# Optimization experiments

Hardware: AMD Instinct MI355X
Metric: run time of the kernel (lower is better)

Reference implementation:

```python
import jax, jax.numpy as jnp
import numpy as np

K = 9          # kernel_size
PAD = 4        # padding
N_OUT, C_IN = 32, 32


def setup_inputs() -> dict:
    key = jax.random.key(0)
    k1, k2, k3, k4, k5 = jax.random.split(key, 5)
    x = jax.random.normal(k1, (16, C_IN, 192, 192), jnp.float32)
    sx = jax.random.uniform(k2, (N_OUT, C_IN), jnp.float32, 0.2, 4.0)
    sy = jax.random.uniform(k3, (N_OUT, C_IN), jnp.float32, 0.2, 4.0)
    th = jax.random.uniform(k4, (N_OUT, C_IN), jnp.float32, 0.0, 2.0 * np.pi)
    weight = jnp.stack([sx, sy, th], axis=-1)          # [N, C, 3]
    bias = jax.random.normal(k5, (N_OUT,), jnp.float32) * 0.01
    return {"x": x, "weight": weight, "bias": bias}


def _gaussian_kernels(weight, k):
    # weight: [N, C, 3] -> normalized anisotropic Gaussian kernels [N, C, k, k]
    sx, sy = weight[..., 0], weight[..., 1]
    rad = weight[..., 2] / 180.0 * jnp.pi          # matches theta/180*pi in source
    c, s = jnp.cos(rad), jnp.sin(rad)
    sx2, sy2 = sx * sx, sy * sy
    # Sigma = U diag(sx^2, sy^2) U^T, U = [[c,-s],[s,c]] -> Sigma = [[a,b],[b,d]]
    a = c * c * sx2 + s * s * sy2
    b = c * s * (sx2 - sy2)
    d = s * s * sx2 + c * c * sy2
    det = a * d - b * b
    ia, ib, id_ = d / det, -b / det, a / det       # closed-form 2x2 inverse
    ax = jnp.arange(k, dtype=jnp.float32) - k // 2
    xx = ax[None, :]                               # x varies along columns
    yy = ax[:, None]                               # y varies along rows
    # quadratic form: ia*x^2 + 2*ib*x*y + id*y^2, broadcast to [N, C, k, k]
    q = (ia[..., None, None] * (xx * xx)
         + 2.0 * ib[..., None, None] * (xx * yy)
         + id_[..., None, None] * (yy * yy))
    ker = jnp.exp(-0.5 * q)
    return ker / jnp.sum(ker, axis=(-2, -1), keepdims=True)


def reference(x, weight, bias):
    w = _gaussian_kernels(weight, K)               # [N, C, K, K]
    out = jax.lax.conv_general_dilated(
        x, w, window_strides=(1, 1), padding=[(PAD, PAD), (PAD, PAD)],
        dimension_numbers=("NCHW", "OIHW", "NCHW"))
    return out + bias[None, :, None, None]
```

## Files before the change

### kernel.cpp

```cpp
#include <hip/hip_runtime.h>

#define H 192
#define W 192
#define CIN 32
#define NOUT 32
#define NB 16
#define PADI 4

#define HT 16
#define WTL 16
#define RROWS 24
#define RCOLS 24

typedef __attribute__((ext_vector_type(8))) short bf16x8;
typedef __attribute__((ext_vector_type(4))) float f32x4;

__device__ __forceinline__ unsigned short f2bf(float f) {
    union { float f; unsigned int u; } v; v.f = f;
    unsigned int r = v.u + 0x7fffu + ((v.u >> 16) & 1u);
    return (unsigned short)(r >> 16);
}

__global__ void genw_kernel(const float* __restrict__ wp, unsigned short* __restrict__ W2g) {
    const int b = blockIdx.x;
    const int o = b >> 5;
    const int i = b & 31;
    const int t = threadIdx.x;

    float sx = wp[b * 3 + 0], sy = wp[b * 3 + 1], th = wp[b * 3 + 2];
    float rad = th / 180.0f * 3.14159265358979323846f;
    float co = cosf(rad), si = sinf(rad);
    float sx2 = sx * sx, sy2 = sy * sy;
    float a = co * co * sx2 + si * si * sy2;
    float bb = co * si * (sx2 - sy2);
    float d = si * si * sx2 + co * co * sy2;
    float det = a * d - bb * bb;
    float ia = d / det, ib = -bb / det, idd = a / det;

    const int tap = t;
    float e = 0.0f;
    if (tap < 81) {
        float xx = (float)(tap % 9 - 4);
        float yy = (float)(tap / 9 - 4);
        float q = ia * xx * xx + 2.0f * ib * xx * yy + idd * yy * yy;
        e = expf(-0.5f * q);
    }
    float s = e;
    #pragma unroll
    for (int off = 32; off > 0; off >>= 1) s += __shfl_down(s, off);
    __shared__ float ws[2];
    if ((t & 63) == 0) ws[t >> 6] = s;
    __syncthreads();
    float total = ws[0] + ws[1];

    if (tap < 81) {
        int mt = o >> 4, m = o & 15, quad = i >> 3, j = i & 7;
        W2g[((((mt * 81 + tap) * 4 + quad) * 16 + m) << 3) + j] = f2bf(e / total);
    }
}

__global__ __launch_bounds__(256, 4) void conv_kernel(
    const float* __restrict__ x, const unsigned short* __restrict__ W2g,
    const float* __restrict__ bias, float* __restrict__ out)
{
    __shared__ __align__(16) unsigned short ldsx[4 * RROWS * RCOLS * 8];

    const int t = threadIdx.x;
    const int bid = (blockIdx.x & 7) * 288 + (blockIdx.x >> 3);
    const int wb = bid % (W / WTL);
    const int hb = (bid / (W / WTL)) % (H / HT);
    const int n  = bid / ((W / WTL) * (H / HT));
    const int row0 = hb * HT - PADI;
    const int col0 = wb * WTL - PADI;
    const float* xn = x + (size_t)n * CIN * H * W;

    float v[9][8];
    #pragma unroll
    for (int it = 0; it < 9; ++it) {
        int idx = it * 256 + t;
        int w = idx % RCOLS;
        int r = (idx / RCOLS) % RROWS;
        int quad = idx / (RCOLS * RROWS);
        int row = row0 + r, col = col0 + w;
        #pragma unroll
        for (int k = 0; k < 8; k++) v[it][k] = 0.0f;
        if ((unsigned)row < (unsigned)H && (unsigned)col < (unsigned)W) {
            const float* p = xn + ((size_t)(quad * 8) * H + row) * W + col;
            #pragma unroll
            for (int k = 0; k < 8; k++) v[it][k] = p[(size_t)k * H * W];
        }
    }
    #pragma unroll
    for (int it = 0; it < 9; ++it) {
        int idx = it * 256 + t;
        unsigned int d[4];
        #pragma unroll
        for (int k = 0; k < 4; k++)
            d[k] = (unsigned int)f2bf(v[it][2 * k]) | ((unsigned int)f2bf(v[it][2 * k + 1]) << 16);
        *(uint4*)&ldsx[(size_t)idx * 8] = make_uint4(d[0], d[1], d[2], d[3]);
    }

    const int wave = t >> 6;
    const int lane = t & 63;
    const int l15 = lane & 15;
    const int quad4 = lane >> 4;
    const int mt = wave & 1;
    const int rbase = (wave >> 1) * 8;

    const bf16x8* __restrict__ Wp = (const bf16x8*)W2g;

    bf16x8 A[2][9];
    #pragma unroll
    for (int dy = 0; dy < 9; dy++)
        A[0][dy] = Wp[((mt * 81 + dy * 9 + 0) * 4 + quad4) * 16 + l15];

    __syncthreads();

    f32x4 acc[8];
    #pragma unroll
    for (int i = 0; i < 8; i++) acc[i] = (f32x4){0.f, 0.f, 0.f, 0.f};

    const unsigned short* bptr = &ldsx[(size_t)(((quad4 * RROWS + rbase) * RCOLS) + l15) * 8];

    #pragma unroll
    for (int dx = 0; dx < 9; dx++) {
        const int cur = dx & 1, nxt = cur ^ 1;
        if (dx < 8) {
            #pragma unroll
            for (int dy = 0; dy < 9; dy++)
                A[nxt][dy] = Wp[((mt * 81 + dy * 9 + (dx + 1)) * 4 + quad4) * 16 + l15];
        }
        #pragma unroll
        for (int rr = 0; rr < 16; rr++) {
            const bf16x8 bfrag = *(const bf16x8*)&bptr[(size_t)(rr * RCOLS + dx) * 8];
            #pragma unroll
            for (int dy = 0; dy < 9; dy++) {
                const int orr = rr - dy;
                if (orr >= 0 && orr < 8) {
                    acc[orr] = __builtin_amdgcn_mfma_f32_16x16x32_bf16(
                        A[cur][dy], bfrag, acc[orr], 0, 0, 0);
                }
            }
        }
    }

    float* outn = out + (size_t)n * NOUT * H * W;
    float bb[4];
    #pragma unroll
    for (int reg = 0; reg < 4; reg++) bb[reg] = bias[mt * 16 + quad4 * 4 + reg];
    #pragma unroll
    for (int orr = 0; orr < 8; orr++) {
        const int row = hb * HT + rbase + orr;
        const int col = wb * WTL + l15;
        #pragma unroll
        for (int reg = 0; reg < 4; reg++) {
            const int och = mt * 16 + quad4 * 4 + reg;
            outn[((size_t)och * H + row) * W + col] = acc[orr][reg] + bb[reg];
        }
    }
}

extern "C" void kernel_launch(void* const* d_in, const int* in_sizes, int n_in,
                              void* d_out, int out_size, void* d_ws, size_t ws_size,
                              hipStream_t stream) {
    const float* x    = (const float*)d_in[0];
    const float* wp   = (const float*)d_in[1];
    const float* bias = (const float*)d_in[2];
    float* out = (float*)d_out;
    unsigned short* W2g = (unsigned short*)d_ws;

    genw_kernel<<<NOUT * CIN, 128, 0, stream>>>(wp, W2g);
    const int blocks = NB * (H / HT) * (W / WTL);
    conv_kernel<<<blocks, 256, 0, stream>>>(x, W2g, bias, out);
}
```

Baseline: 190.2 us.

## Pre-pad and convert input to bf16 NHWC, load tiles via global_load_lds

A new prep kernel converts the fp32 NCHW input into a zero-padded bf16 channel-interleaved buffer in workspace, and also generates the Gaussian weights in the same launch. The conv kernel then fills LDS with direct global-to-LDS 16-byte loads, with no bounds checks or per-tile conversion. This removes the repeated halo reads and fp32-to-bf16 conversion done in every tile. In exchange it adds an extra full pass over the input and roughly 41 MB of workspace writes and reads. The old path remains as a fallback when the workspace is too small.

Result: no change. 192.5 us (+1.2%).

```diff
diff --git a/kernel.cpp b/kernel.cpp
--- a/kernel.cpp
+++ b/kernel.cpp
@@ -1,4 +1,5 @@
 #include <hip/hip_runtime.h>
+#include <stdint.h>
 
 #define H 192
 #define W 192
@@ -9,11 +10,15 @@
 
 #define HT 16
 #define WTL 16
-#define RROWS 24
-#define RCOLS 24
+#define RR 24
+#define RC 24
+#define PADW 200
 
 typedef __attribute__((ext_vector_type(8))) short bf16x8;
 typedef __attribute__((ext_vector_type(4))) float f32x4;
+
+typedef __attribute__((address_space(1))) const void gvoid;
+typedef __attribute__((address_space(3))) void svoid;
 
 __device__ __forceinline__ unsigned short f2bf(float f) {
     union { float f; unsigned int u; } v; v.f = f;
@@ -21,12 +26,12 @@
     return (unsigned short)(r >> 16);
 }
 
-__global__ void genw_kernel(const float* __restrict__ wp, unsigned short* __restrict__ W2g) {
-    const int b = blockIdx.x;
+__device__ __forceinline__ void genw_body(int b, int t, int nthr,
+                                          const float* __restrict__ wp,
+                                          unsigned short* __restrict__ W2g,
+                                          float* ws ) {
     const int o = b >> 5;
     const int i = b & 31;
-    const int t = threadIdx.x;
-
     float sx = wp[b * 3 + 0], sy = wp[b * 3 + 1], th = wp[b * 3 + 2];
     float rad = th / 180.0f * 3.14159265358979323846f;
     float co = cosf(rad), si = sinf(rad);
@@ -48,10 +53,10 @@
     float s = e;
     #pragma unroll
     for (int off = 32; off > 0; off >>= 1) s += __shfl_down(s, off);
-    __shared__ float ws[2];
     if ((t & 63) == 0) ws[t >> 6] = s;
     __syncthreads();
-    float total = ws[0] + ws[1];
+    float total = 0.0f;
+    for (int k = 0; k < nthr / 64; k++) total += ws[k];
 
     if (tap < 81) {
         int mt = o >> 4, m = o & 15, quad = i >> 3, j = i & 7;
@@ -59,11 +64,131 @@
     }
 }
 
+__global__ void prep_kernel(const float* __restrict__ x, const float* __restrict__ wp,
+                            unsigned short* __restrict__ W2g,
+                            unsigned short* __restrict__ xpad) {
+    __shared__ float ws[4];
+    if (blockIdx.x < 10000) {
+        int gid = blockIdx.x * 256 + threadIdx.x;
+        int q = gid & 3;
+        int pix = gid >> 2;
+        int pw = pix % PADW;
+        int rest = pix / PADW;
+        int pr = rest % PADW;
+        int n = rest / PADW;
+        int r = pr - PADI, c = pw - PADI;
+        unsigned int d[4] = {0u, 0u, 0u, 0u};
+        if ((unsigned)r < (unsigned)H && (unsigned)c < (unsigned)W) {
+            const float* p = x + (((size_t)n * CIN + q * 8) * H + r) * W + c;
+            #pragma unroll
+            for (int k = 0; k < 4; k++) {
+                float v0 = p[(size_t)(2 * k) * H * W];
+                float v1 = p[(size_t)(2 * k + 1) * H * W];
+                d[k] = (unsigned int)f2bf(v0) | ((unsigned int)f2bf(v1) << 16);
+            }
+        }
+        *(uint4*)(xpad + (size_t)gid * 8) = make_uint4(d[0], d[1], d[2], d[3]);
+    } else {
+        genw_body(blockIdx.x - 10000, threadIdx.x, 256, wp, W2g, ws);
+    }
+}
+
+__global__ void genw_kernel(const float* __restrict__ wp, unsigned short* __restrict__ W2g) {
+    __shared__ float ws[2];
+    genw_body(blockIdx.x, threadIdx.x, 128, wp, W2g, ws);
+}
+
 __global__ __launch_bounds__(256, 4) void conv_kernel(
+    const unsigned short* __restrict__ xpad, const unsigned short* __restrict__ W2g,
+    const float* __restrict__ bias, float* __restrict__ out)
+{
+    __shared__ __align__(16) unsigned short ldsx[4 * RR * RC * 8];
+
+    const int t = threadIdx.x;
+    const int bid = (blockIdx.x & 7) * 288 + (blockIdx.x >> 3);
+    const int wb = bid % (W / WTL);
+    const int hb = (bid / (W / WTL)) % (H / HT);
+    const int n  = bid / ((W / WTL) * (H / HT));
+    const int wave = t >> 6;
+    const int lane = t & 63;
+
+    {
+        const size_t pixbase = ((size_t)n * PADW + hb * HT) * PADW + wb * WTL;
+        const unsigned short* srcq = xpad + pixbase * 32 + wave * 8;
+        #pragma unroll
+        for (int k = 0; k < 9; k++) {
+            int rem = k * 64 + lane;
+            int r = rem / RC;
+            int w = rem - r * RC;
+            const unsigned short* src = srcq + ((size_t)r * PADW + w) * 32;
+            char* dst = (char*)ldsx + ((size_t)(wave * 576 + k * 64) * 16);
+            __builtin_amdgcn_global_load_lds((gvoid*)src, (svoid*)dst, 16, 0, 0);
+        }
+    }
+
+    const int l15 = lane & 15;
+    const int quad4 = lane >> 4;
+    const int mt = wave & 1;
+    const int rbase = (wave >> 1) * 8;
+
+    const bf16x8* __restrict__ Wp = (const bf16x8*)W2g;
+
+    bf16x8 A[2][9];
+    #pragma unroll
+    for (int dy = 0; dy < 9; dy++)
+        A[0][dy] = Wp[((mt * 81 + dy * 9 + 0) * 4 + quad4) * 16 + l15];
+
+    __syncthreads();
+
+    f32x4 acc[8];
+    #pragma unroll
+    for (int i = 0; i < 8; i++) acc[i] = (f32x4){0.f, 0.f, 0.f, 0.f};
+
+    const unsigned short* bptr = &ldsx[(size_t)(((quad4 * RR + rbase) * RC) + l15) * 8];
+
+    #pragma unroll
+    for (int dx = 0; dx < 9; dx++) {
+        const int cur = dx & 1, nxt = cur ^ 1;
+        if (dx < 8) {
+            #pragma unroll
+            for (int dy = 0; dy < 9; dy++)
+                A[nxt][dy] = Wp[((mt * 81 + dy * 9 + (dx + 1)) * 4 + quad4) * 16 + l15];
+        }
+        #pragma unroll
+        for (int rr = 0; rr < 16; rr++) {
+            const bf16x8 bfrag = *(const bf16x8*)&bptr[(size_t)(rr * RC + dx) * 8];
+            #pragma unroll
+            for (int dy = 0; dy < 9; dy++) {
+                const int orr = rr - dy;
+                if (orr >= 0 && orr < 8) {
+                    acc[orr] = __builtin_amdgcn_mfma_f32_16x16x32_bf16(
+                        A[cur][dy], bfrag, acc[orr], 0, 0, 0);
+                }
+            }
+        }
+    }
+
+    float* outn = out + (size_t)n * NOUT * H * W;
+    float bb[4];
+    #pragma unroll
+    for (int reg = 0; reg < 4; reg++) bb[reg] = bias[mt * 16 + quad4 * 4 + reg];
+    #pragma unroll
+    for (int orr = 0; orr < 8; orr++) {
+        const int row = hb * HT + rbase + orr;
+        const int col = wb * WTL + l15;
+        #pragma unroll
+        for (int reg = 0; reg < 4; reg++) {
+            const int och = mt * 16 + quad4 * 4 + reg;
+            outn[((size_t)och * H + row) * W + col] = acc[orr][reg] + bb[reg];
+        }
+    }
+}
+
+__global__ __launch_bounds__(256, 4) void conv_fb(
     const float* __restrict__ x, const unsigned short* __restrict__ W2g,
     const float* __restrict__ bias, float* __restrict__ out)
 {
-    __shared__ __align__(16) unsigned short ldsx[4 * RROWS * RCOLS * 8];
+    __shared__ __align__(16) unsigned short ldsx[4 * RR * RC * 8];
 
     const int t = threadIdx.x;
     const int bid = (blockIdx.x & 7) * 288 + (blockIdx.x >> 3);
@@ -78,9 +203,9 @@
     #pragma unroll
     for (int it = 0; it < 9; ++it) {
         int idx = it * 256 + t;
-        int w = idx % RCOLS;
-        int r = (idx / RCOLS) % RROWS;
-        int quad = idx / (RCOLS * RROWS);
+        int w = idx % RC;
+        int r = (idx / RC) % RR;
+        int quad = idx / (RC * RR);
         int row = row0 + r, col = col0 + w;
         #pragma unroll
         for (int k = 0; k < 8; k++) v[it][k] = 0.0f;
@@ -108,7 +233,6 @@
     const int rbase = (wave >> 1) * 8;
 
     const bf16x8* __restrict__ Wp = (const bf16x8*)W2g;
-
     bf16x8 A[2][9];
     #pragma unroll
     for (int dy = 0; dy < 9; dy++)
@@ -120,7 +244,7 @@
     #pragma unroll
     for (int i = 0; i < 8; i++) acc[i] = (f32x4){0.f, 0.f, 0.f, 0.f};
 
-    const unsigned short* bptr = &ldsx[(size_t)(((quad4 * RROWS + rbase) * RCOLS) + l15) * 8];
+    const unsigned short* bptr = &ldsx[(size_t)(((quad4 * RR + rbase) * RC) + l15) * 8];
 
     #pragma unroll
     for (int dx = 0; dx < 9; dx++) {
@@ -132,7 +256,7 @@
         }
         #pragma unroll
         for (int rr = 0; rr < 16; rr++) {
-            const bf16x8 bfrag = *(const bf16x8*)&bptr[(size_t)(rr * RCOLS + dx) * 8];
+            const bf16x8 bfrag = *(const bf16x8*)&bptr[(size_t)(rr * RC + dx) * 8];
             #pragma unroll
             for (int dy = 0; dy < 9; dy++) {
                 const int orr = rr - dy;
@@ -167,9 +291,19 @@
     const float* wp   = (const float*)d_in[1];
     const float* bias = (const float*)d_in[2];
     float* out = (float*)d_out;
-    unsigned short* W2g = (unsigned short*)d_ws;
-
-    genw_kernel<<<NOUT * CIN, 128, 0, stream>>>(wp, W2g);
+
+    const size_t W2G_BYTES  = 165888;
+    const size_t XPAD_BYTES = (size_t)NB * PADW * PADW * CIN * 2;
+
+    unsigned short* W2g  = (unsigned short*)d_ws;
     const int blocks = NB * (H / HT) * (W / WTL);
-    conv_kernel<<<blocks, 256, 0, stream>>>(x, W2g, bias, out);
-}
+
+    if (ws_size >= W2G_BYTES + XPAD_BYTES) {
+        unsigned short* xpad = (unsigned short*)((char*)d_ws + W2G_BYTES);
+        prep_kernel<<<11024, 256, 0, stream>>>(x, wp, W2g, xpad);
+        conv_kernel<<<blocks, 256, 0, stream>>>(xpad, W2g, bias, out);
+    } else {
+        genw_kernel<<<NOUT * CIN, 128, 0, stream>>>(wp, W2g);
+        conv_fb<<<blocks, 256, 0, stream>>>(x, W2g, bias, out);
+    }
+}
```
